# Kernel optimization log

Hardware: AMD Instinct MI355X
Metric: run time of the kernel (lower is better)

The kernel has to match this reference:

```python
import jax, jax.numpy as jnp
import numpy as np

B, S, D = 2, 2048, 1024
H = 16
HD = D // H

def setup_inputs() -> dict:
    key = jax.random.key(0)
    k1, k2, k3 = jax.random.split(key, 3)
    # xavier-uniform-ish scale for weights
    x = jax.random.normal(k1, (B, S, D), dtype=jnp.float32)
    lim_qkv = np.sqrt(6.0 / (D + 3 * D)).astype(np.float32)
    lim_o = np.sqrt(6.0 / (D + D)).astype(np.float32)
    qkv_w = jax.random.uniform(k2, (3 * D, D), minval=-lim_qkv, maxval=lim_qkv, dtype=jnp.float32)
    o_w = jax.random.uniform(k3, (D, D), minval=-lim_o, maxval=lim_o, dtype=jnp.float32)
    qkv_b = jnp.zeros((3 * D,), dtype=jnp.float32)
    o_b = jnp.zeros((D,), dtype=jnp.float32)
    return {"x": x, "qkv_w": qkv_w, "qkv_b": qkv_b, "o_w": o_w, "o_b": o_b}

def reference(x, qkv_w, qkv_b, o_w, o_b):
    b, s, _ = x.shape
    # qkv projection: Linear(input_dim, 3*embed_dim)
    qkv = jnp.einsum('bsd,ed->bse', x, qkv_w) + qkv_b          # [B,S,3D]
    qkv = qkv.reshape(b, s, H, 3 * HD).transpose(0, 2, 1, 3)    # [B,H,S,3*HD]
    q, k, v = jnp.split(qkv, 3, axis=-1)                        # each [B,H,S,HD]
    scale = 1.0 / np.sqrt(HD).astype(np.float32)
    scores = jnp.einsum('bhqd,bhkd->bhqk', q, k) * scale        # [B,H,S,S]
    attn = jax.nn.softmax(scores, axis=-1)
    vals = jnp.einsum('bhqk,bhkd->bhqd', attn, v)               # [B,H,S,HD]
    vals = vals.transpose(0, 2, 1, 3).reshape(b, s, H * HD)     # [B,S,D]
    o = jnp.einsum('bse,de->bsd', vals, o_w) + o_b              # [B,S,D]
    return o
```

## Files before the change

### kernel.cpp

```cpp
#include <hip/hip_runtime.h>
#include <math.h>
#include <stdint.h>

typedef _Float16 half_t;
typedef _Float16 f16x8 __attribute__((ext_vector_type(8)));
typedef _Float16 f16x4 __attribute__((ext_vector_type(4)));
typedef _Float16 f16x2 __attribute__((ext_vector_type(2)));
typedef __fp16   fp16x2 __attribute__((ext_vector_type(2)));
typedef float    f32x4 __attribute__((ext_vector_type(4)));
typedef float    f32x16 __attribute__((ext_vector_type(16)));
typedef unsigned int u32x2 __attribute__((ext_vector_type(2)));

__device__ __forceinline__ void gload16(const void* g, void* l) {
    __builtin_amdgcn_global_load_lds(
        (const __attribute__((address_space(1))) void*)(uintptr_t)g,
        (__attribute__((address_space(3))) void*)(uint32_t)(uintptr_t)l,
        16, 0, 0);
}

__device__ __forceinline__ float fast_exp2(float x) {
#if __has_builtin(__builtin_amdgcn_exp2f)
    return __builtin_amdgcn_exp2f(x);
#else
    return exp2f(x);
#endif
}
__device__ __forceinline__ unsigned cvt2h_u32(float a, float b) {
#if __has_builtin(__builtin_amdgcn_cvt_pkrtz)
    union { fp16x2 s; unsigned d; } u;
    u.s = __builtin_amdgcn_cvt_pkrtz(a, b);
    return u.d;
#else
    union { f16x2 s; unsigned d; } u;
    u.s = (f16x2){ (half_t)a, (half_t)b };
    return u.d;
#endif
}

#define QSCALE 0.18033688011112042f

__global__ __launch_bounds__(256)
void cvt3_kernel(const float* __restrict__ a, half_t* __restrict__ da, int na,
                 const float* __restrict__ b, half_t* __restrict__ db, int nb,
                 const float* __restrict__ c, half_t* __restrict__ dc, int nc)
{
    const int total = na + nb + nc;
    for (int i = blockIdx.x * 256 + threadIdx.x; i < total; i += gridDim.x * 256) {
        const float* s; half_t* d; int off;
        if (i < na)           { s = a; d = da; off = i; }
        else if (i < na + nb) { s = b; d = db; off = i - na; }
        else                  { s = c; d = dc; off = i - na - nb; }
        float4 v = reinterpret_cast<const float4*>(s)[off];
        f16x4 h = { (half_t)v.x, (half_t)v.y, (half_t)v.z, (half_t)v.w };
        reinterpret_cast<f16x4*>(d)[off] = h;
    }
}

template<int BM, int BN, int MODE, int MINWG, int DBUF>
__global__ __launch_bounds__(256, MINWG)
void gemm_kernel(const half_t* __restrict__ A,
                 const half_t* __restrict__ Bw,
                 const float* __restrict__ bias,
                 void* __restrict__ outp,
                 half_t* __restrict__ kout,
                 half_t* __restrict__ vtout,
                 int N, int K, int nbx)
{
    constexpr int CA = BM / 32, CB = BN / 32;
    constexpr int MW = BM / 2,  NW = BN / 2;
    constexpr int IF = MW / 16, JF = NW / 16;
    constexpr int AE = BM * 64, BE = BN * 64;
    constexpr int NB = DBUF ? 2 : 1;

    __shared__ half_t As[NB * AE];
    __shared__ half_t Bs[NB * BE];

    const int tid  = threadIdx.x;
    const int lane = tid & 63;
    const int w    = tid >> 6;
    const int wm   = w >> 1, wn = w & 1;
    const int lr   = lane & 15, lg = lane >> 4;
    const int swk  = lr & 7;

    const int nwg = gridDim.x;
    const int cpx = nwg >> 3;
    const int swz = (blockIdx.x & 7) * cpx + (blockIdx.x >> 3);
    const int m0  = (swz % nbx) * BM;
    const int n0  = (swz / nbx) * BN;

    const int srow = lane >> 3;
    const int scol = ((lane & 7) ^ srow) * 8;

    f32x4 acc[JF][IF] = {};

    if constexpr (!DBUF) {
        for (int k0 = 0; k0 < K; k0 += 64) {
            #pragma unroll
            for (int c = 0; c < CA; ++c) {
                const int chunk = w * CA + c;
                const int row   = chunk * 8 + srow;
                gload16(&A[(size_t)(m0 + row) * K + k0 + scol], &As[chunk * 512]);
            }
            #pragma unroll
            for (int c = 0; c < CB; ++c) {
                const int chunk = w * CB + c;
                const int row   = chunk * 8 + srow;
                gload16(&Bw[(size_t)(n0 + row) * K + k0 + scol], &Bs[chunk * 512]);
            }
            __syncthreads();

            #pragma unroll
            for (int kk = 0; kk < 2; ++kk) {
                f16x8 af[IF], bf[JF];
                #pragma unroll
                for (int i = 0; i < IF; ++i)
                    af[i] = *reinterpret_cast<const f16x8*>(
                        &As[(wm*MW + i*16 + lr) * 64 + (((kk*4 + lg) ^ swk) << 3)]);
                #pragma unroll
                for (int j = 0; j < JF; ++j)
                    bf[j] = *reinterpret_cast<const f16x8*>(
                        &Bs[(wn*NW + j*16 + lr) * 64 + (((kk*4 + lg) ^ swk) << 3)]);
                #pragma unroll
                for (int j = 0; j < JF; ++j)
                    #pragma unroll
                    for (int i = 0; i < IF; ++i)
                        acc[j][i] = __builtin_amdgcn_mfma_f32_16x16x32_f16(bf[j], af[i], acc[j][i], 0, 0, 0);
            }
            __syncthreads();
        }
    } else {
        const int NT = K >> 6;
        #pragma unroll
        for (int c = 0; c < CA; ++c) {
            const int chunk = w * CA + c;
            const int row   = chunk * 8 + srow;
            gload16(&A[(size_t)(m0 + row) * K + scol], &As[chunk * 512]);
        }
        #pragma unroll
        for (int c = 0; c < CB; ++c) {
            const int chunk = w * CB + c;
            const int row   = chunk * 8 + srow;
            gload16(&Bw[(size_t)(n0 + row) * K + scol], &Bs[chunk * 512]);
        }
        __syncthreads();

        int cur = 0;
        for (int kt = 0; kt < NT; ++kt) {
            if (kt + 1 < NT) {
                const int k1 = (kt + 1) << 6;
                #pragma unroll
                for (int c = 0; c < CA; ++c) {
                    const int chunk = w * CA + c;
                    const int row   = chunk * 8 + srow;
                    gload16(&A[(size_t)(m0 + row) * K + k1 + scol], &As[(cur ^ 1) * AE + chunk * 512]);
                }
                #pragma unroll
                for (int c = 0; c < CB; ++c) {
                    const int chunk = w * CB + c;
                    const int row   = chunk * 8 + srow;
                    gload16(&Bw[(size_t)(n0 + row) * K + k1 + scol], &Bs[(cur ^ 1) * BE + chunk * 512]);
                }
            }
            #pragma unroll
            for (int kk = 0; kk < 2; ++kk) {
                f16x8 af[IF], bf[JF];
                #pragma unroll
                for (int i = 0; i < IF; ++i)
                    af[i] = *reinterpret_cast<const f16x8*>(
                        &As[cur * AE + (wm*MW + i*16 + lr) * 64 + (((kk*4 + lg) ^ swk) << 3)]);
                #pragma unroll
                for (int j = 0; j < JF; ++j)
                    bf[j] = *reinterpret_cast<const f16x8*>(
                        &Bs[cur * BE + (wn*NW + j*16 + lr) * 64 + (((kk*4 + lg) ^ swk) << 3)]);
                #pragma unroll
                for (int j = 0; j < JF; ++j)
                    #pragma unroll
                    for (int i = 0; i < IF; ++i)
                        acc[j][i] = __builtin_amdgcn_mfma_f32_16x16x32_f16(bf[j], af[i], acc[j][i], 0, 0, 0);
            }
            if (kt + 1 < NT) __syncthreads();
            cur ^= 1;
        }
    }

    #pragma unroll
    for (int j = 0; j < JF; ++j) {
        const int nb = n0 + wn*NW + j*16 + lg*4;
        const float4 bv = *reinterpret_cast<const float4*>(&bias[nb]);
        #pragma unroll
        for (int i = 0; i < IF; ++i) {
            const int gm = m0 + wm*MW + i*16 + lr;
            f32x4 v = acc[j][i];
            v[0] += bv.x; v[1] += bv.y; v[2] += bv.z; v[3] += bv.w;
            if (MODE == 1) {
                float4 st = { v[0], v[1], v[2], v[3] };
                *reinterpret_cast<float4*>(&((float*)outp)[(size_t)gm * N + nb]) = st;
            } else {
                const int b = gm >> 11, s = gm & 2047;
                const int h = nb / 192, cc = nb % 192;
                const int t = cc >> 6, d = cc & 63;
                const size_t bh = (size_t)(b * 16 + h);
                if (t == 0) {
                    f16x4 hv = { (half_t)(v[0]*QSCALE), (half_t)(v[1]*QSCALE),
                                 (half_t)(v[2]*QSCALE), (half_t)(v[3]*QSCALE) };
                    *reinterpret_cast<f16x4*>(&((half_t*)outp)[(bh*2048 + s)*64 + d]) = hv;
                } else if (t == 1) {
                    f16x4 hv = { (half_t)v[0], (half_t)v[1], (half_t)v[2], (half_t)v[3] };
                    *reinterpret_cast<f16x4*>(&kout[(bh*2048 + s)*64 + d]) = hv;
                } else {
                    #pragma unroll
                    for (int r = 0; r < 4; ++r)
                        vtout[(bh*64 + d + r)*2048 + s] = (half_t)v[r];
                }
            }
        }
    }
}

__global__ __launch_bounds__(512, 2)
void attn_kernel(const half_t* __restrict__ qb,
                 const half_t* __restrict__ kb,
                 const half_t* __restrict__ vtb,
                 half_t* __restrict__ vals)
{
    __shared__ __attribute__((aligned(16))) char buf[49152];
    half_t* KtH = (half_t*)buf;
    half_t* VtH = (half_t*)(buf + 24576);

    const int tid  = threadIdx.x;
    const int lane = tid & 63;
    const int w    = tid >> 6;
    const int wq   = w & 3;
    const int kh   = w >> 2;
    const int q32  = lane & 31;
    const int hi   = lane >> 5;
    const int i    = blockIdx.x;
    const int bh   = (i & 7) * 4 + ((i >> 3) & 3);
    const int qblk = i >> 5;
    const int b    = bh >> 4, h = bh & 15;
    const size_t base = (size_t)bh * 2048 * 64;
    const int q0 = qblk * 128;
    const int swk = lane & 7;

    f16x8 qf[4];
    {
        const int qr = q0 + wq*32 + q32;
        #pragma unroll
        for (int kd = 0; kd < 4; ++kd)
            qf[kd] = *reinterpret_cast<const f16x8*>(&qb[base + (size_t)qr*64 + kd*16 + hi*8]);
    }

    const int srow = tid >> 3;
    const int ssl  = (tid & 7) ^ (srow & 7);
    const half_t* kg = kb  + base + (size_t)srow * 64   + ssl * 8;
    const half_t* vg = vtb + base + (size_t)srow * 2048 + ssl * 8;
    const int ldst = w * 512;

    f32x16 acco[2] = {};
    float l_run = 0.0f;

    #pragma unroll
    for (int tt = 0; tt < 3; ++tt) {
        gload16(kg + (size_t)tt * 4096, &KtH[tt * 4096 + ldst]);
        gload16(vg + tt * 64,           &VtH[tt * 4096 + ldst]);
    }

    int bi = 0;
    for (int t = 0; t < 32; ++t) {
        const int rem = 31 - t;
        if (rem >= 2)      asm volatile("s_waitcnt vmcnt(4)" ::: "memory");
        else if (rem == 1) asm volatile("s_waitcnt vmcnt(2)" ::: "memory");
        else               asm volatile("s_waitcnt vmcnt(0)" ::: "memory");
        __builtin_amdgcn_s_barrier();
        __builtin_amdgcn_sched_barrier(0);

        const half_t* Kc = &KtH[bi * 4096];
        const half_t* Vc = &VtH[bi * 4096];

        f32x16 accs = {};
        __builtin_amdgcn_s_setprio(1);
        #pragma unroll
        for (int kd = 0; kd < 4; ++kd) {
            const f16x8 kf = *reinterpret_cast<const f16x8*>(
                &Kc[(kh*32 + q32) * 64 + (((kd*2 + hi) ^ swk) << 3)]);
            accs = __builtin_amdgcn_mfma_f32_32x32x16_f16(kf, qf[kd], accs, 0, 0, 0);
        }
        __builtin_amdgcn_s_setprio(0);

        unsigned P2[8];
        float psum = 0.0f;
        #pragma unroll
        for (int p = 0; p < 8; ++p) {
            const float pa = fast_exp2(accs[2*p]);
            const float pb = fast_exp2(accs[2*p+1]);
            psum += pa + pb;
            P2[p] = cvt2h_u32(pa, pb);
        }
        l_run += psum;

        __builtin_amdgcn_s_setprio(1);
        #pragma unroll
        for (int kb2 = 0; kb2 < 2; ++kb2) {
            const u32x2 s0 = __builtin_amdgcn_permlane32_swap(P2[4*kb2+0], P2[4*kb2+2], false, false);
            const u32x2 s1 = __builtin_amdgcn_permlane32_swap(P2[4*kb2+1], P2[4*kb2+3], false, false);
            union { unsigned u[4]; f16x8 v; } pf;
            pf.u[0] = s0[0]; pf.u[1] = s1[0]; pf.u[2] = s0[1]; pf.u[3] = s1[1];
            #pragma unroll
            for (int d2 = 0; d2 < 2; ++d2) {
                const f16x8 vf = *reinterpret_cast<const f16x8*>(
                    &Vc[(d2*32 + q32) * 64 + (((kh*4 + kb2*2 + hi) ^ swk) << 3)]);
                acco[d2] = __builtin_amdgcn_mfma_f32_32x32x16_f16(vf, pf.v, acco[d2], 0, 0, 0);
            }
        }
        __builtin_amdgcn_s_setprio(0);

        __builtin_amdgcn_s_barrier();
        if (t < 29) {
            gload16(kg + (size_t)(t + 3) * 4096, &KtH[bi * 4096 + ldst]);
            gload16(vg + (t + 3) * 64,           &VtH[bi * 4096 + ldst]);
        }
        bi = (bi == 2) ? 0 : bi + 1;
    }

    l_run += __shfl_xor(l_run, 32);

    float* mrg = (float*)buf;
    __syncthreads();
    if (kh == 1) {
        float* dst = &mrg[(wq*64 + lane) * 33];
        #pragma unroll
        for (int d2 = 0; d2 < 2; ++d2)
            #pragma unroll
            for (int r = 0; r < 16; ++r) dst[d2*16 + r] = acco[d2][r];
        dst[32] = l_run;
    }
    __syncthreads();
    if (kh == 0) {
        const float* src = &mrg[(wq*64 + lane) * 33];
        const float inv_l = 1.0f / (l_run + src[32]);
        const int row = b*2048 + q0 + wq*32 + q32;
        #pragma unroll
        for (int d2 = 0; d2 < 2; ++d2) {
            #pragma unroll
            for (int rq = 0; rq < 4; ++rq) {
                const int dbase = d2*32 + rq*8 + hi*4;
                f16x4 hv;
                #pragma unroll
                for (int j = 0; j < 4; ++j) {
                    const int r = rq*4 + j;
                    hv[j] = (half_t)((acco[d2][r] + src[d2*16 + r]) * inv_l);
                }
                *reinterpret_cast<f16x4*>(&vals[(size_t)row*1024 + h*64 + dbase]) = hv;
            }
        }
    }
}

extern "C" void kernel_launch(void* const* d_in, const int* in_sizes, int n_in,
                              void* d_out, int out_size, void* d_ws, size_t ws_size,
                              hipStream_t stream)
{
    const float* x     = (const float*)d_in[0];
    const float* qkv_w = (const float*)d_in[1];
    const float* qkv_b = (const float*)d_in[2];
    const float* o_w   = (const float*)d_in[3];
    const float* o_b   = (const float*)d_in[4];
    float* out = (float*)d_out;

    const size_t M1 = (size_t)1024 * 1024;
    half_t* x16   = (half_t*)d_ws;
    half_t* w16   = x16   + 4 * M1;
    half_t* ow16  = w16   + 3 * M1;
    half_t* qbuf  = ow16  + 1 * M1;
    half_t* kbuf  = qbuf  + 4 * M1;
    half_t* vtbuf = kbuf  + 4 * M1;
    half_t* vals  = vtbuf + 4 * M1;

    cvt3_kernel<<<2048, 256, 0, stream>>>(x, x16, 1048576, qkv_w, w16, 786432, o_w, ow16, 262144);
    gemm_kernel<128, 128, 0, 3, 0><<<768, 256, 0, stream>>>(
        x16, w16, qkv_b, qbuf, kbuf, vtbuf, 3072, 1024, 32);
    attn_kernel<<<512, 512, 0, stream>>>(qbuf, kbuf, vtbuf, vals);
    gemm_kernel<128, 64, 1, 2, 1><<<512, 256, 0, stream>>>(
        vals, ow16, o_b, out, nullptr, nullptr, 1024, 1024, 32);
}
```

Baseline: 101.4 us.

## Load K and V fragments directly from global memory instead of LDS staging

```diff
diff --git a/kernel.cpp b/kernel.cpp
--- a/kernel.cpp
+++ b/kernel.cpp
@@ -223,9 +223,7 @@
                  const half_t* __restrict__ vtb,
                  half_t* __restrict__ vals)
 {
-    __shared__ __attribute__((aligned(16))) char buf[49152];
-    half_t* KtH = (half_t*)buf;
-    half_t* VtH = (half_t*)(buf + 24576);
+    __shared__ float mrg[4 * 64 * 33];
 
     const int tid  = threadIdx.x;
     const int lane = tid & 63;
@@ -240,7 +238,6 @@
     const int b    = bh >> 4, h = bh & 15;
     const size_t base = (size_t)bh * 2048 * 64;
     const int q0 = qblk * 128;
-    const int swk = lane & 7;
 
     f16x8 qf[4];
     {
@@ -250,41 +247,31 @@
             qf[kd] = *reinterpret_cast<const f16x8*>(&qb[base + (size_t)qr*64 + kd*16 + hi*8]);
     }
 
-    const int srow = tid >> 3;
-    const int ssl  = (tid & 7) ^ (srow & 7);
-    const half_t* kg = kb  + base + (size_t)srow * 64   + ssl * 8;
-    const half_t* vg = vtb + base + (size_t)srow * 2048 + ssl * 8;
-    const int ldst = w * 512;
+    const half_t* kp = kb  + base + (size_t)(kh*32 + q32) * 64 + hi*8;
+    const half_t* vp = vtb + base + kh*32 + hi*8;
 
     f32x16 acco[2] = {};
     float l_run = 0.0f;
 
-    #pragma unroll
-    for (int tt = 0; tt < 3; ++tt) {
-        gload16(kg + (size_t)tt * 4096, &KtH[tt * 4096 + ldst]);
-        gload16(vg + tt * 64,           &VtH[tt * 4096 + ldst]);
-    }
-
-    int bi = 0;
+    #pragma unroll 2
     for (int t = 0; t < 32; ++t) {
-        const int rem = 31 - t;
-        if (rem >= 2)      asm volatile("s_waitcnt vmcnt(4)" ::: "memory");
-        else if (rem == 1) asm volatile("s_waitcnt vmcnt(2)" ::: "memory");
-        else               asm volatile("s_waitcnt vmcnt(0)" ::: "memory");
-        __builtin_amdgcn_s_barrier();
-        __builtin_amdgcn_sched_barrier(0);
-
-        const half_t* Kc = &KtH[bi * 4096];
-        const half_t* Vc = &VtH[bi * 4096];
+        f16x8 kf[4];
+        #pragma unroll
+        for (int kd = 0; kd < 4; ++kd)
+            kf[kd] = *reinterpret_cast<const f16x8*>(&kp[(size_t)t*4096 + kd*16]);
+        f16x8 vf[4];
+        #pragma unroll
+        for (int d2 = 0; d2 < 2; ++d2)
+            #pragma unroll
+            for (int kb2 = 0; kb2 < 2; ++kb2)
+                vf[d2*2 + kb2] = *reinterpret_cast<const f16x8*>(
+                    &vp[(size_t)(d2*32 + q32)*2048 + t*64 + kb2*16]);
 
         f32x16 accs = {};
         __builtin_amdgcn_s_setprio(1);
         #pragma unroll
-        for (int kd = 0; kd < 4; ++kd) {
-            const f16x8 kf = *reinterpret_cast<const f16x8*>(
-                &Kc[(kh*32 + q32) * 64 + (((kd*2 + hi) ^ swk) << 3)]);
-            accs = __builtin_amdgcn_mfma_f32_32x32x16_f16(kf, qf[kd], accs, 0, 0, 0);
-        }
+        for (int kd = 0; kd < 4; ++kd)
+            accs = __builtin_amdgcn_mfma_f32_32x32x16_f16(kf[kd], qf[kd], accs, 0, 0, 0);
         __builtin_amdgcn_s_setprio(0);
 
         unsigned P2[8];
@@ -306,25 +293,14 @@
             union { unsigned u[4]; f16x8 v; } pf;
             pf.u[0] = s0[0]; pf.u[1] = s1[0]; pf.u[2] = s0[1]; pf.u[3] = s1[1];
             #pragma unroll
-            for (int d2 = 0; d2 < 2; ++d2) {
-                const f16x8 vf = *reinterpret_cast<const f16x8*>(
-                    &Vc[(d2*32 + q32) * 64 + (((kh*4 + kb2*2 + hi) ^ swk) << 3)]);
-                acco[d2] = __builtin_amdgcn_mfma_f32_32x32x16_f16(vf, pf.v, acco[d2], 0, 0, 0);
-            }
+            for (int d2 = 0; d2 < 2; ++d2)
+                acco[d2] = __builtin_amdgcn_mfma_f32_32x32x16_f16(vf[d2*2 + kb2], pf.v, acco[d2], 0, 0, 0);
         }
         __builtin_amdgcn_s_setprio(0);
-
-        __builtin_amdgcn_s_barrier();
-        if (t < 29) {
-            gload16(kg + (size_t)(t + 3) * 4096, &KtH[bi * 4096 + ldst]);
-            gload16(vg + (t + 3) * 64,           &VtH[bi * 4096 + ldst]);
-        }
-        bi = (bi == 2) ? 0 : bi + 1;
     }
 
     l_run += __shfl_xor(l_run, 32);
 
-    float* mrg = (float*)buf;
     __syncthreads();
     if (kh == 1) {
         float* dst = &mrg[(wq*64 + lane) * 33];
```

New measurement: 175.1 us. 1.73x slower.
